# Optimization experiments

Measured on AMD Instinct MI355X. Metric: run time of the kernel, lower is better.

The kernel has to match this reference:

```python
import jax, jax.numpy as jnp
import numpy as np

EPS = 1e-08

def setup_inputs() -> dict:
    key = jax.random.key(0)
    k1, k2 = jax.random.split(key)
    h = jax.random.normal(k1, (4, 4096, 2048), dtype=jnp.float32)
    vectors = jax.random.normal(k2, (16, 2048), dtype=jnp.float32) * 0.01
    return {"h": h, "vectors": vectors}

def reference(h, vectors):
    # Chain of k Householder reflections applied sequentially (loop-carried h).
    def step(h, v):
        v_norm_sq = jnp.maximum(jnp.dot(v, v), EPS)
        proj = jnp.einsum('bsd,d->bs', h, v)  # [B,S]
        h = h - (2.0 / v_norm_sq) * proj[..., None] * v
        return h, None
    h, _ = jax.lax.scan(step, h, vectors)
    return h
```

## Files before the change

### kernel.cpp

```cpp
#include <hip/hip_runtime.h>

#define HH_EPS 1e-8f

constexpr int D     = 2048;
constexpr int K     = 16;
constexpr int RR    = 2;
constexpr int CH    = D / (64 * 4);
constexpr int NROWS = 4 * 4096;
constexpr int WPB   = 4;
constexpr int SPAD  = 17;

__global__ void __launch_bounds__(64) hh_gram_kernel(const float* __restrict__ vecs,
                                                     float* __restrict__ G) {
    int i = blockIdx.x >> 4, j = blockIdx.x & 15;
    int lane = threadIdx.x;
    const float4* a = (const float4*)(vecs + i * D);
    const float4* b = (const float4*)(vecs + j * D);
    float s = 0.f;
#pragma unroll
    for (int c = 0; c < CH; ++c) {
        float4 x = a[c * 64 + lane], y = b[c * 64 + lane];
        s += x.x * y.x + x.y * y.y + x.z * y.z + x.w * y.w;
    }
#pragma unroll
    for (int off = 32; off >= 1; off >>= 1) s += __shfl_xor(s, off);
    if (lane == 0) G[i * K + j] = s;
}

__global__ void __launch_bounds__(256) hh_buildT_kernel(const float* __restrict__ G,
                                                        float* __restrict__ T) {
    __shared__ float sG[K * K], sT[K * K];
    int t = threadIdx.x;
    sG[t] = G[t]; sT[t] = 0.f;
    __syncthreads();
    for (int k = 0; k < K; ++k) {
        float beta = 2.f / fmaxf(sG[k * K + k], HH_EPS);
        if (t == k) sT[k * K + k] = beta;
        else if (t < k) {
            float s = 0.f;
            for (int j = t; j < k; ++j) s += sT[t * K + j] * sG[j * K + k];
            sT[t * K + k] = -beta * s;
        }
        __syncthreads();
    }
    T[t] = sT[t];
}

__device__ __forceinline__ void wy_dot_phase(const float4 (&h)[RR][CH],
                                             float4 (&va)[CH],
                                             const float4* __restrict__ v4,
                                             int knext, int lane,
                                             float* __restrict__ myP, int k) {
    float a0x = 0.f, a0y = 0.f, a0z = 0.f, a0w = 0.f;
    float a1x = 0.f, a1y = 0.f, a1z = 0.f, a1w = 0.f;
#pragma unroll
    for (int j = 0; j < CH; ++j) {
        float4 v = va[j];
        a0x += h[0][j].x * v.x; a0y += h[0][j].y * v.y;
        a0z += h[0][j].z * v.z; a0w += h[0][j].w * v.w;
        a1x += h[1][j].x * v.x; a1y += h[1][j].y * v.y;
        a1z += h[1][j].z * v.z; a1w += h[1][j].w * v.w;
        va[j] = v4[knext * (D / 4) + j * 64 + lane];
    }
    float s0 = (a0x + a0y) + (a0z + a0w);
    float s1 = (a1x + a1y) + (a1z + a1w);
    s0 += __shfl_xor(s0, 32); s0 += __shfl_xor(s0, 16);
    s1 += __shfl_xor(s1, 32); s1 += __shfl_xor(s1, 16);
    if (lane < 16) {
        myP[(0 * K + k) * SPAD + lane] = s0;
        myP[(1 * K + k) * SPAD + lane] = s1;
    }
}

__device__ __forceinline__ void wy_upd_phase(float4 (&h)[RR][CH],
                                             float4 (&va)[CH],
                                             const float4* __restrict__ v4,
                                             int knext, int lane,
                                             float w0, float w1) {
#pragma unroll
    for (int j = 0; j < CH; ++j) {
        float4 v = va[j];
        h[0][j].x -= w0 * v.x; h[0][j].y -= w0 * v.y;
        h[0][j].z -= w0 * v.z; h[0][j].w -= w0 * v.w;
        h[1][j].x -= w1 * v.x; h[1][j].y -= w1 * v.y;
        h[1][j].z -= w1 * v.z; h[1][j].w -= w1 * v.w;
        va[j] = v4[knext * (D / 4) + j * 64 + lane];
    }
}

__global__ void __launch_bounds__(256, 4)
hh_apply_wy(const float* __restrict__ h_in, const float* __restrict__ vecs,
            const float* __restrict__ Tmat, float* __restrict__ h_out) {
    __shared__ float sP[WPB * RR * K * SPAD];
    __shared__ float sD[WPB * RR * K];
    __shared__ float sW[WPB * RR * K];
    __shared__ float sT[K * K];

    const int t    = threadIdx.x;
    const int wv   = t >> 6;
    const int lane = t & 63;
    const int gw   = blockIdx.x * WPB + wv;
    const size_t rbase = (size_t)gw * RR;

    float4 h[RR][CH];
    const float4* hin4 = (const float4*)h_in;
#pragma unroll
    for (int r = 0; r < RR; ++r)
#pragma unroll
        for (int j = 0; j < CH; ++j)
            h[r][j] = hin4[(rbase + r) * (D / 4) + j * 64 + lane];

    const float4* v4 = (const float4*)vecs;
    float4 va[CH];
#pragma unroll
    for (int j = 0; j < CH; ++j) va[j] = v4[j * 64 + lane];

    sT[t] = Tmat[t];
    __syncthreads();

    float* myP = sP + wv * (RR * K * SPAD);
    float* myD = sD + wv * (RR * K);
    float* myW = sW + wv * (RR * K);

#pragma unroll 1
    for (int k = 0; k < K; ++k)
        wy_dot_phase(h, va, v4, (k + 1) & 15, lane, myP, k);

    const int kk  = lane & 15;
    const int seg = lane >> 4;
#pragma unroll
    for (int r = 0; r < RR; ++r) {
        float s = 0.f;
#pragma unroll
        for (int i = 0; i < 4; ++i)
            s += myP[(r * K + kk) * SPAD + seg * 4 + i];
        s += __shfl_xor(s, 16);
        s += __shfl_xor(s, 32);
        if (lane < 16) myD[r * K + kk] = s;
    }

#pragma unroll
    for (int r = 0; r < RR; ++r) {
        float wsum = 0.f;
#pragma unroll
        for (int k2 = 0; k2 < K; ++k2)
            wsum += myD[r * K + k2] * sT[k2 * K + kk];
        if (lane < 16) myW[r * K + kk] = wsum;
    }

#pragma unroll 1
    for (int k = 0; k < K; ++k) {
        float w0 = myW[0 * K + k];
        float w1 = myW[1 * K + k];
        wy_upd_phase(h, va, v4, (k + 1) & 15, lane, w0, w1);
    }

#pragma unroll
    for (int r = 0; r < RR; ++r) {
        float4* row = (float4*)h_out + (rbase + r) * (D / 4);
#pragma unroll
        for (int j = 0; j < CH; ++j)
            row[j * 64 + lane] = h[r][j];
    }
}

extern "C" void kernel_launch(void* const* d_in, const int* in_sizes, int n_in,
                              void* d_out, int out_size, void* d_ws, size_t ws_size,
                              hipStream_t stream) {
    const float* h    = (const float*)d_in[0];
    const float* vecs = (const float*)d_in[1];
    float* out        = (float*)d_out;

    float* G  = (float*)d_ws;
    float* Tm = G + K * K;

    hh_gram_kernel<<<K * K, 64, 0, stream>>>(vecs, G);
    hh_buildT_kernel<<<1, 256, 0, stream>>>(G, Tm);

    int blocks = NROWS / (RR * WPB);
    hh_apply_wy<<<blocks, 256, 0, stream>>>(h, vecs, Tm, out);
}
```

Baseline: 297.8 us.

## Stage all Householder vectors in LDS per 1024-thread block

The apply kernel now copies all 16 Householder vectors (128KB) into shared memory once per block using direct global-to-LDS loads. Previously every wave streamed the vectors from global memory or cache twice, once in the dot phase and once in the update phase. Blocks grow to 1024 threads (16 waves) so that one staged copy is shared by more rows, and the cross-lane reduction layout is adjusted to fit. The large LDS footprint limits each CU to one block, which lowers occupancy and exposes the initial staging latency before any compute starts.

```diff
diff --git a/kernel.cpp b/kernel.cpp
--- a/kernel.cpp
+++ b/kernel.cpp
@@ -7,8 +7,9 @@
 constexpr int RR    = 2;
 constexpr int CH    = D / (64 * 4);
 constexpr int NROWS = 4 * 4096;
-constexpr int WPB   = 4;
-constexpr int SPAD  = 17;
+constexpr int TPB   = 1024;
+constexpr int WPB   = TPB / 64;
+constexpr int SPAD  = 9;
 
 __global__ void __launch_bounds__(64) hh_gram_kernel(const float* __restrict__ vecs,
                                                      float* __restrict__ G) {
@@ -46,55 +47,14 @@
     T[t] = sT[t];
 }
 
-__device__ __forceinline__ void wy_dot_phase(const float4 (&h)[RR][CH],
-                                             float4 (&va)[CH],
-                                             const float4* __restrict__ v4,
-                                             int knext, int lane,
-                                             float* __restrict__ myP, int k) {
-    float a0x = 0.f, a0y = 0.f, a0z = 0.f, a0w = 0.f;
-    float a1x = 0.f, a1y = 0.f, a1z = 0.f, a1w = 0.f;
-#pragma unroll
-    for (int j = 0; j < CH; ++j) {
-        float4 v = va[j];
-        a0x += h[0][j].x * v.x; a0y += h[0][j].y * v.y;
-        a0z += h[0][j].z * v.z; a0w += h[0][j].w * v.w;
-        a1x += h[1][j].x * v.x; a1y += h[1][j].y * v.y;
-        a1z += h[1][j].z * v.z; a1w += h[1][j].w * v.w;
-        va[j] = v4[knext * (D / 4) + j * 64 + lane];
-    }
-    float s0 = (a0x + a0y) + (a0z + a0w);
-    float s1 = (a1x + a1y) + (a1z + a1w);
-    s0 += __shfl_xor(s0, 32); s0 += __shfl_xor(s0, 16);
-    s1 += __shfl_xor(s1, 32); s1 += __shfl_xor(s1, 16);
-    if (lane < 16) {
-        myP[(0 * K + k) * SPAD + lane] = s0;
-        myP[(1 * K + k) * SPAD + lane] = s1;
-    }
-}
-
-__device__ __forceinline__ void wy_upd_phase(float4 (&h)[RR][CH],
-                                             float4 (&va)[CH],
-                                             const float4* __restrict__ v4,
-                                             int knext, int lane,
-                                             float w0, float w1) {
-#pragma unroll
-    for (int j = 0; j < CH; ++j) {
-        float4 v = va[j];
-        h[0][j].x -= w0 * v.x; h[0][j].y -= w0 * v.y;
-        h[0][j].z -= w0 * v.z; h[0][j].w -= w0 * v.w;
-        h[1][j].x -= w1 * v.x; h[1][j].y -= w1 * v.y;
-        h[1][j].z -= w1 * v.z; h[1][j].w -= w1 * v.w;
-        va[j] = v4[knext * (D / 4) + j * 64 + lane];
-    }
-}
-
-__global__ void __launch_bounds__(256, 4)
+__global__ void __launch_bounds__(1024, 4)
 hh_apply_wy(const float* __restrict__ h_in, const float* __restrict__ vecs,
             const float* __restrict__ Tmat, float* __restrict__ h_out) {
-    __shared__ float sP[WPB * RR * K * SPAD];
-    __shared__ float sD[WPB * RR * K];
-    __shared__ float sW[WPB * RR * K];
-    __shared__ float sT[K * K];
+    __shared__ float4 sv[K * (D / 4)];
+    __shared__ float  sP[WPB * RR * K * SPAD];
+    __shared__ float  sD[WPB * RR * K];
+    __shared__ float  sW[WPB * RR * K];
+    __shared__ float  sT[K * K];
 
     const int t    = threadIdx.x;
     const int wv   = t >> 6;
@@ -111,11 +71,15 @@
             h[r][j] = hin4[(rbase + r) * (D / 4) + j * 64 + lane];
 
     const float4* v4 = (const float4*)vecs;
-    float4 va[CH];
 #pragma unroll
-    for (int j = 0; j < CH; ++j) va[j] = v4[j * 64 + lane];
-
-    sT[t] = Tmat[t];
+    for (int i = 0; i < K * (D / 4) / TPB; ++i) {
+        int idx = t + i * TPB;
+        __builtin_amdgcn_global_load_lds(
+            (const __attribute__((address_space(1))) unsigned int*)(v4 + idx),
+            (__attribute__((address_space(3))) unsigned int*)(sv + idx),
+            16, 0, 0);
+    }
+    if (t < K * K) sT[t] = Tmat[t];
     __syncthreads();
 
     float* myP = sP + wv * (RR * K * SPAD);
@@ -123,17 +87,33 @@
     float* myW = sW + wv * (RR * K);
 
 #pragma unroll 1
-    for (int k = 0; k < K; ++k)
-        wy_dot_phase(h, va, v4, (k + 1) & 15, lane, myP, k);
+    for (int k = 0; k < K; ++k) {
+        float a0x = 0.f, a0y = 0.f, a0z = 0.f, a0w = 0.f;
+        float a1x = 0.f, a1y = 0.f, a1z = 0.f, a1w = 0.f;
+#pragma unroll
+        for (int j = 0; j < CH; ++j) {
+            float4 v = sv[k * (D / 4) + j * 64 + lane];
+            a0x += h[0][j].x * v.x; a0y += h[0][j].y * v.y;
+            a0z += h[0][j].z * v.z; a0w += h[0][j].w * v.w;
+            a1x += h[1][j].x * v.x; a1y += h[1][j].y * v.y;
+            a1z += h[1][j].z * v.z; a1w += h[1][j].w * v.w;
+        }
+        float s0 = (a0x + a0y) + (a0z + a0w);
+        float s1 = (a1x + a1y) + (a1z + a1w);
+        s0 += __shfl_xor(s0, 32); s0 += __shfl_xor(s0, 16); s0 += __shfl_xor(s0, 8);
+        s1 += __shfl_xor(s1, 32); s1 += __shfl_xor(s1, 16); s1 += __shfl_xor(s1, 8);
+        if (lane < 8) {
+            myP[(0 * K + k) * SPAD + lane] = s0;
+            myP[(1 * K + k) * SPAD + lane] = s1;
+        }
+    }
 
     const int kk  = lane & 15;
     const int seg = lane >> 4;
 #pragma unroll
     for (int r = 0; r < RR; ++r) {
-        float s = 0.f;
-#pragma unroll
-        for (int i = 0; i < 4; ++i)
-            s += myP[(r * K + kk) * SPAD + seg * 4 + i];
+        float s = myP[(r * K + kk) * SPAD + seg * 2]
+                + myP[(r * K + kk) * SPAD + seg * 2 + 1];
         s += __shfl_xor(s, 16);
         s += __shfl_xor(s, 32);
         if (lane < 16) myD[r * K + kk] = s;
@@ -150,9 +130,16 @@
 
 #pragma unroll 1
     for (int k = 0; k < K; ++k) {
-        float w0 = myW[0 * K + k];
-        float w1 = myW[1 * K + k];
-        wy_upd_phase(h, va, v4, (k + 1) & 15, lane, w0, w1);
+        const float w0 = myW[0 * K + k];
+        const float w1 = myW[1 * K + k];
+#pragma unroll
+        for (int j = 0; j < CH; ++j) {
+            float4 v = sv[k * (D / 4) + j * 64 + lane];
+            h[0][j].x -= w0 * v.x; h[0][j].y -= w0 * v.y;
+            h[0][j].z -= w0 * v.z; h[0][j].w -= w0 * v.w;
+            h[1][j].x -= w1 * v.x; h[1][j].y -= w1 * v.y;
+            h[1][j].z -= w1 * v.z; h[1][j].w -= w1 * v.w;
+        }
     }
 
 #pragma unroll
@@ -178,5 +165,5 @@
     hh_buildT_kernel<<<1, 256, 0, stream>>>(G, Tm);
 
     int blocks = NROWS / (RR * WPB);
-    hh_apply_wy<<<blocks, 256, 0, stream>>>(h, vecs, Tm, out);
+    hh_apply_wy<<<blocks, TPB, 0, stream>>>(h, vecs, Tm, out);
 }
```

After: 261.8 us. 12.1% less time.
